# Optimization experiments

Hardware: AMD Instinct MI355X
Metric: run time of the kernel (lower is better)

Reference implementation:

```python
import jax, jax.numpy as jnp
import numpy as np

ENC_DIM = 256
DEC_HIDDEN = 128


def _lstm_cell(x, h, c, W_ih, W_hh, b_ih, b_hh):
    # gates: [B, 4H], PyTorch LSTMCell gate order: i, f, g, o
    gates = x @ W_ih.T + b_ih + h @ W_hh.T + b_hh
    i, f, g, o = jnp.split(gates, 4, axis=-1)
    i = jax.nn.sigmoid(i)
    f = jax.nn.sigmoid(f)
    g = jnp.tanh(g)
    o = jax.nn.sigmoid(o)
    c_new = f * c + i * g
    h_new = o * jnp.tanh(c_new)
    return h_new, c_new


def setup_inputs() -> dict:
    key = jax.random.key(0)
    ks = jax.random.split(key, 12)
    B, L, E, H = 256, 512, ENC_DIM, DEC_HIDDEN
    s_e = 1.0 / np.sqrt(H)
    inp = {
        "hist_ctx": jax.random.normal(ks[0], (B, L, E), dtype=jnp.float32),
        "fut_ctx": jax.random.normal(ks[1], (B, L, E), dtype=jnp.float32),
        "W_ih_h": jax.random.uniform(ks[2], (4 * H, E), jnp.float32, -s_e, s_e),
        "W_hh_h": jax.random.uniform(ks[3], (4 * H, H), jnp.float32, -s_e, s_e),
        "b_ih_h": jax.random.uniform(ks[4], (4 * H,), jnp.float32, -s_e, s_e),
        "b_hh_h": jax.random.uniform(ks[5], (4 * H,), jnp.float32, -s_e, s_e),
        "W_ih_f": jax.random.uniform(ks[6], (4 * H, E), jnp.float32, -s_e, s_e),
        "W_hh_f": jax.random.uniform(ks[7], (4 * H, H), jnp.float32, -s_e, s_e),
        "b_ih_f": jax.random.uniform(ks[8], (4 * H,), jnp.float32, -s_e, s_e),
        "b_hh_f": jax.random.uniform(ks[9], (4 * H,), jnp.float32, -s_e, s_e),
        "W_ffn": jax.random.uniform(ks[10], (1, 2 * H), jnp.float32, -1.0 / np.sqrt(2 * H), 1.0 / np.sqrt(2 * H)),
        "b_ffn": jax.random.uniform(ks[11], (1,), jnp.float32, -1.0 / np.sqrt(2 * H), 1.0 / np.sqrt(2 * H)),
    }
    return inp


def reference(hist_ctx, fut_ctx, W_ih_h, W_hh_h, b_ih_h, b_hh_h,
              W_ih_f, W_hh_f, b_ih_f, b_hh_f, W_ffn, b_ffn):
    B, L, _ = hist_ctx.shape
    H = W_hh_h.shape[1]
    h0 = jnp.zeros((B, H), dtype=hist_ctx.dtype)
    init = (h0, h0, h0, h0)  # h_h, c_h, h_f, c_f

    # time-major inputs for scan: [L, B, E]
    xs = (jnp.swapaxes(hist_ctx, 0, 1), jnp.swapaxes(fut_ctx, 0, 1))

    def step(carry, x):
        h_h, c_h, h_f, c_f = carry
        x_h, x_f = x
        h_h, c_h = _lstm_cell(x_h, h_h, c_h, W_ih_h, W_hh_h, b_ih_h, b_hh_h)
        h_f, c_f = _lstm_cell(x_f, h_f, c_f, W_ih_f, W_hh_f, b_ih_f, b_hh_f)
        comb = jnp.concatenate([h_h, h_f], axis=-1)  # [B, 2H]
        y_t = (comb @ W_ffn.T + b_ffn)[:, 0]          # [B]
        return (h_h, c_h, h_f, c_f), y_t

    _, ys = jax.lax.scan(step, init, xs)  # ys: [L, B]
    return jnp.swapaxes(ys, 0, 1)         # [B, L]
```

## Files before the change

### kernel.cpp

```cpp
#include <hip/hip_runtime.h>

#define B_ 256
#define L_ 512
#define E_ 256
#define H_ 128
#define G4_ 512
#define TC 16
#define NCH 32

typedef _Float16 half8  __attribute__((ext_vector_type(8)));
typedef float   float4v __attribute__((ext_vector_type(4)));
typedef int     int4v   __attribute__((ext_vector_type(4)));
typedef unsigned int uint32;

static constexpr size_t WT_OFF = 0;
static constexpr size_t WT_SZ  = (size_t)2 * 8 * 512 * 32 * 2;
static constexpr size_t WH_OFF = WT_OFF + WT_SZ;
static constexpr size_t WH_SZ  = (size_t)2 * 2 * 4 * 512 * 32 * 2;
static constexpr size_t YP_OFF = WH_OFF + WH_SZ;
static constexpr size_t YP_SZ  = (size_t)B_ * L_ * 4;
static constexpr size_t WS_NEEDED = YP_OFF + YP_SZ;

__device__ __forceinline__ int pk16(float lo, float hi) {
  return __builtin_bit_cast(int, __builtin_amdgcn_cvt_pkrtz(lo, hi));
}
__device__ __forceinline__ float sigf(float x) {
  return __builtin_amdgcn_rcpf(1.f + __builtin_amdgcn_exp2f(-1.44269504f * x));
}
__device__ __forceinline__ float tanhf_(float x) {
  return 1.f - 2.f * __builtin_amdgcn_rcpf(1.f + __builtin_amdgcn_exp2f(2.88539008f * x));
}

__global__ void prep(const float* __restrict__ WihH, const float* __restrict__ WihF,
                     const float* __restrict__ WhhH, const float* __restrict__ WhhF,
                     unsigned char* __restrict__ ws) {
  int id = blockIdx.x * 256 + threadIdx.x;
  if (id < 262144) {
    int lstm = id >> 17;
    int r = id & 131071;
    int kc = r >> 14;
    int r2 = r & 16383;
    int n = r2 >> 5, k5 = r2 & 31;
    const float* src = lstm ? WihF : WihH;
    ((_Float16*)(ws + WT_OFF))[id] = (_Float16)src[n * E_ + kc * 32 + k5];
  } else {
    int id2 = id - 262144;
    int lstm = id2 >> 17;
    int r = id2 & 131071;
    int sel = r >> 16;
    int r2 = r & 65535;
    int kc = r2 >> 14;
    int r3 = r2 & 16383;
    int n = r3 >> 5, k5 = r3 & 31;
    const float* src = lstm ? WhhF : WhhH;
    float wv = src[n * H_ + kc * 32 + k5];
    _Float16 hi = (_Float16)wv;
    _Float16 o = sel ? (_Float16)((wv - (float)hi) * 4096.f) : hi;
    ((_Float16*)(ws + WH_OFF))[id2] = o;
  }
}

__global__ __launch_bounds__(512, 2) void fused(
    const float* __restrict__ Xh, const float* __restrict__ Xf,
    const float* __restrict__ bihH, const float* __restrict__ bhhH,
    const float* __restrict__ bihF, const float* __restrict__ bhhF,
    const float* __restrict__ Wffn, unsigned char* __restrict__ ws,
    float* __restrict__ out) {
  const int bp = blockIdx.x, lstm = blockIdx.y;
  const int tid = threadIdx.x;
  const int w = tid >> 6, lane = tid & 63, quad = lane >> 4, l15 = lane & 15;
  __shared__ float GxL[TC * 2 * 512];
  __shared__ _Float16 hA2[2][512];
  __shared__ float hist[TC * 2 * 128];
  __shared__ float ybuf[2 * 512];

  const int u = w * 16 + l15;
  const int gk = u >> 3, jj = u & 7;
  const unsigned char* WH = ws + WH_OFF;
  half8 whh[2][4][4];
#pragma unroll
  for (int sel = 0; sel < 2; ++sel)
#pragma unroll
    for (int nt = 0; nt < 4; ++nt)
#pragma unroll
      for (int kc = 0; kc < 4; ++kc) {
        size_t byte =
            (size_t)(((lstm * 2 + sel) * 4 + kc) * 512 + (nt * 128 + u)) * 64 + quad * 16;
        whh[sel][nt][kc] = *(const half8*)(WH + byte);
      }
  float bias4[4];
#pragma unroll
  for (int nt = 0; nt < 4; ++nt) {
    int g = nt * 128 + u;
    bias4[nt] = lstm ? (bihF[g] + bhhF[g]) : (bihH[g] + bhhH[g]);
  }
  const float wf0 = Wffn[lstm * 128 + 2 * lane];
  const float wf1 = Wffn[lstm * 128 + 2 * lane + 1];
  const float* Xb0 = (lstm ? Xf : Xh) + (size_t)(2 * bp) * L_ * E_;
  const float* Xb1 = Xb0 + (size_t)L_ * E_;
  const unsigned char* WT = ws + WT_OFF + (size_t)lstm * 262144;
  float* yp1 = (float*)(ws + YP_OFF);
  float* ypout = (lstm == 0) ? (out + (size_t)(2 * bp) * L_) : (yp1 + (size_t)(2 * bp) * L_);

  float cst = 0.f;
  const float s_lo = 1.f / 4096.f;

  for (int ch = 0; ch < NCH; ++ch) {
    float4v ax[2][4];
#pragma unroll
    for (int mt = 0; mt < 2; ++mt)
#pragma unroll
      for (int nt = 0; nt < 4; ++nt) ax[mt][nt] = (float4v){0.f, 0.f, 0.f, 0.f};
#pragma unroll 2
    for (int kc = 0; kc < 8; ++kc) {
      const float* xa0 = Xb0 + (size_t)(ch * TC + l15) * E_ + kc * 32 + quad * 8;
      const float* xa1 = Xb1 + (size_t)(ch * TC + l15) * E_ + kc * 32 + quad * 8;
      float4v u0 = *(const float4v*)xa0, u1 = *(const float4v*)(xa0 + 4);
      float4v v0 = *(const float4v*)xa1, v1 = *(const float4v*)(xa1 + 4);
      int4v ai;
      ai[0] = pk16(u0[0], u0[1]); ai[1] = pk16(u0[2], u0[3]);
      ai[2] = pk16(u1[0], u1[1]); ai[3] = pk16(u1[2], u1[3]);
      half8 A0 = __builtin_bit_cast(half8, ai);
      ai[0] = pk16(v0[0], v0[1]); ai[1] = pk16(v0[2], v0[3]);
      ai[2] = pk16(v1[0], v1[1]); ai[3] = pk16(v1[2], v1[3]);
      half8 A1 = __builtin_bit_cast(half8, ai);
#pragma unroll
      for (int nt = 0; nt < 4; ++nt) {
        const unsigned char* bptr =
            WT + (size_t)kc * 32768 + (size_t)(nt * 128 + u) * 64 + quad * 16;
        half8 bf = *(const half8*)bptr;
        ax[0][nt] = __builtin_amdgcn_mfma_f32_16x16x32_f16(A0, bf, ax[0][nt], 0, 0, 0);
        ax[1][nt] = __builtin_amdgcn_mfma_f32_16x16x32_f16(A1, bf, ax[1][nt], 0, 0, 0);
      }
    }
#pragma unroll
    for (int mt = 0; mt < 2; ++mt)
#pragma unroll
      for (int nt = 0; nt < 4; ++nt) {
        int colg = nt * 128 + u;
        float bb = bias4[nt];
#pragma unroll
        for (int rg = 0; rg < 4; ++rg)
          GxL[((quad * 4 + rg) * 2 + mt) * 512 + colg] = ax[mt][nt][rg] + bb;
      }
    __syncthreads();

    for (int tl = 0; tl < TC; ++tl) {
      const int st = ch * TC + tl;
      const float* gp = &GxL[(tl * 2 + (quad & 1)) * 512 + u];
      float gx0 = gp[0], gx1 = gp[128], gx2 = gp[256], gx3 = gp[384];

      float4v r1[4], r2[4];
      if (st) {
        const _Float16* hAr = hA2[st & 1];
        half8 hfr[4];
#pragma unroll
        for (int kc = 0; kc < 4; ++kc)
          hfr[kc] = *(const half8*)&hAr[((kc * 4 + quad) * 4 + (l15 & 3)) * 8];
        const float4v z = (float4v){0.f, 0.f, 0.f, 0.f};
#pragma unroll
        for (int nt = 0; nt < 4; ++nt) {
          r1[nt] = __builtin_amdgcn_mfma_f32_16x16x32_f16(hfr[0], whh[0][nt][0], z, 0, 0, 0);
          r2[nt] = __builtin_amdgcn_mfma_f32_16x16x32_f16(hfr[0], whh[1][nt][0], z, 0, 0, 0);
        }
#pragma unroll
        for (int kc = 1; kc < 4; ++kc)
#pragma unroll
          for (int nt = 0; nt < 4; ++nt) {
            r1[nt] = __builtin_amdgcn_mfma_f32_16x16x32_f16(hfr[kc], whh[0][nt][kc], r1[nt], 0, 0, 0);
            r2[nt] = __builtin_amdgcn_mfma_f32_16x16x32_f16(hfr[kc], whh[1][nt][kc], r2[nt], 0, 0, 0);
          }
      } else {
#pragma unroll
        for (int nt = 0; nt < 4; ++nt) {
          r1[nt] = (float4v){0.f, 0.f, 0.f, 0.f};
          r2[nt] = (float4v){0.f, 0.f, 0.f, 0.f};
        }
      }
      if (quad < 2) {
        const int b = quad;
        const bool q1 = (b != 0);
        float p0 = (q1 ? r1[0][1] : r1[0][0]) + s_lo * ((q1 ? r1[0][3] : r1[0][2]) + (q1 ? r2[0][1] : r2[0][0])) + gx0;
        float p1 = (q1 ? r1[1][1] : r1[1][0]) + s_lo * ((q1 ? r1[1][3] : r1[1][2]) + (q1 ? r2[1][1] : r2[1][0])) + gx1;
        float p2 = (q1 ? r1[2][1] : r1[2][0]) + s_lo * ((q1 ? r1[2][3] : r1[2][2]) + (q1 ? r2[2][1] : r2[2][0])) + gx2;
        float p3 = (q1 ? r1[3][1] : r1[3][0]) + s_lo * ((q1 ? r1[3][3] : r1[3][2]) + (q1 ? r2[3][1] : r2[3][0])) + gx3;
        float iv = sigf(p0), fv = sigf(p1);
        float gg = tanhf_(p2), ov = sigf(p3);
        cst = fv * cst + iv * gg;
        float h = ov * tanhf_(cst);
        _Float16 hh = (_Float16)h;
        _Float16 hl = (_Float16)((h - (float)hh) * 4096.f);
        _Float16* hAw = hA2[(st + 1) & 1];
        hAw[(gk * 4 + b) * 8 + jj] = hh;
        hAw[(gk * 4 + 2 + b) * 8 + jj] = hl;
        hist[(tl * 2 + b) * 128 + u] = h;
      }
      __syncthreads();
    }

#pragma unroll
    for (int i = 0; i < 4; ++i) {
      int d = w * 4 + i;
      int tl = d >> 1, b = d & 1;
      float y = wf0 * hist[(tl * 2 + b) * 128 + 2 * lane] +
                wf1 * hist[(tl * 2 + b) * 128 + 2 * lane + 1];
      y += __shfl_xor(y, 1);
      y += __shfl_xor(y, 2);
      y += __shfl_xor(y, 4);
      y += __shfl_xor(y, 8);
      y += __shfl_xor(y, 16);
      y += __shfl_xor(y, 32);
      if (lane == 0) ybuf[b * 512 + ch * TC + tl] = y;
    }
    __syncthreads();
  }
  ypout[tid] = ybuf[tid];
  ypout[512 + tid] = ybuf[512 + tid];
}

__global__ __launch_bounds__(256) void combine(const unsigned char* __restrict__ ws,
                                               const float* __restrict__ bffn,
                                               float* __restrict__ out) {
  int i = blockIdx.x * 256 + threadIdx.x;
  const float* yp1 = (const float*)(ws + YP_OFF);
  out[i] = out[i] + yp1[i] + bffn[0];
}

extern "C" void kernel_launch(void* const* d_in, const int* in_sizes, int n_in,
                              void* d_out, int out_size, void* d_ws, size_t ws_size,
                              hipStream_t stream) {
  (void)in_sizes; (void)n_in; (void)out_size;
  const float* histX = (const float*)d_in[0];
  const float* futX  = (const float*)d_in[1];
  const float* WihH  = (const float*)d_in[2];
  const float* WhhH  = (const float*)d_in[3];
  const float* bihH  = (const float*)d_in[4];
  const float* bhhH  = (const float*)d_in[5];
  const float* WihF  = (const float*)d_in[6];
  const float* WhhF  = (const float*)d_in[7];
  const float* bihF  = (const float*)d_in[8];
  const float* bhhF  = (const float*)d_in[9];
  const float* Wffn  = (const float*)d_in[10];
  const float* bffn  = (const float*)d_in[11];
  unsigned char* ws = (unsigned char*)d_ws;
  float* out = (float*)d_out;

  if (ws_size < WS_NEEDED) return;

  prep<<<2048, 256, 0, stream>>>(WihH, WihF, WhhH, WhhF, ws);
  fused<<<dim3(B_ / 2, 2), 512, 0, stream>>>(histX, futX, bihH, bhhH, bihF, bhhF, Wffn, ws, out);
  combine<<<512, 256, 0, stream>>>(ws, bffn, out);
}
```

Baseline: 976.9 us.

## Software-pipeline next chunk's input projection into the recurrent timestep loop

The input-projection GEMM for chunk ch+1 is now spread across the 16 recurrent timesteps of chunk ch. Even steps issue the global loads for X and W_ih, and odd steps run the MFMAs, so the load latency and MFMA work hide behind the serial recurrence instead of stalling before each chunk. The GxL buffer gains a padded row stride (513) to reduce LDS bank conflicts. Launch bounds drop to one block per SM, which frees registers for the extra accumulators and prefetch buffers but lowers occupancy.

```diff
diff --git a/kernel.cpp b/kernel.cpp
--- a/kernel.cpp
+++ b/kernel.cpp
@@ -7,6 +7,7 @@
 #define G4_ 512
 #define TC 16
 #define NCH 32
+#define LDG 513
 
 typedef _Float16 half8  __attribute__((ext_vector_type(8)));
 typedef float   float4v __attribute__((ext_vector_type(4)));
@@ -60,7 +61,7 @@
   }
 }
 
-__global__ __launch_bounds__(512, 2) void fused(
+__global__ __launch_bounds__(512, 1) void fused(
     const float* __restrict__ Xh, const float* __restrict__ Xf,
     const float* __restrict__ bihH, const float* __restrict__ bhhH,
     const float* __restrict__ bihF, const float* __restrict__ bhhF,
@@ -69,7 +70,7 @@
   const int bp = blockIdx.x, lstm = blockIdx.y;
   const int tid = threadIdx.x;
   const int w = tid >> 6, lane = tid & 63, quad = lane >> 4, l15 = lane & 15;
-  __shared__ float GxL[TC * 2 * 512];
+  __shared__ float GxL[32 * LDG];
   __shared__ _Float16 hA2[2][512];
   __shared__ float hist[TC * 2 * 128];
   __shared__ float ybuf[2 * 512];
@@ -105,16 +106,16 @@
   float cst = 0.f;
   const float s_lo = 1.f / 4096.f;
 
-  for (int ch = 0; ch < NCH; ++ch) {
-    float4v ax[2][4];
+  {
+    float4v ax0[2][4];
 #pragma unroll
     for (int mt = 0; mt < 2; ++mt)
 #pragma unroll
-      for (int nt = 0; nt < 4; ++nt) ax[mt][nt] = (float4v){0.f, 0.f, 0.f, 0.f};
+      for (int nt = 0; nt < 4; ++nt) ax0[mt][nt] = (float4v){0.f, 0.f, 0.f, 0.f};
 #pragma unroll 2
     for (int kc = 0; kc < 8; ++kc) {
-      const float* xa0 = Xb0 + (size_t)(ch * TC + l15) * E_ + kc * 32 + quad * 8;
-      const float* xa1 = Xb1 + (size_t)(ch * TC + l15) * E_ + kc * 32 + quad * 8;
+      const float* xa0 = Xb0 + (size_t)l15 * E_ + kc * 32 + quad * 8;
+      const float* xa1 = Xb1 + (size_t)l15 * E_ + kc * 32 + quad * 8;
       float4v u0 = *(const float4v*)xa0, u1 = *(const float4v*)(xa0 + 4);
       float4v v0 = *(const float4v*)xa1, v1 = *(const float4v*)(xa1 + 4);
       int4v ai;
@@ -129,8 +130,8 @@
         const unsigned char* bptr =
             WT + (size_t)kc * 32768 + (size_t)(nt * 128 + u) * 64 + quad * 16;
         half8 bf = *(const half8*)bptr;
-        ax[0][nt] = __builtin_amdgcn_mfma_f32_16x16x32_f16(A0, bf, ax[0][nt], 0, 0, 0);
-        ax[1][nt] = __builtin_amdgcn_mfma_f32_16x16x32_f16(A1, bf, ax[1][nt], 0, 0, 0);
+        ax0[0][nt] = __builtin_amdgcn_mfma_f32_16x16x32_f16(A0, bf, ax0[0][nt], 0, 0, 0);
+        ax0[1][nt] = __builtin_amdgcn_mfma_f32_16x16x32_f16(A1, bf, ax0[1][nt], 0, 0, 0);
       }
     }
 #pragma unroll
@@ -141,13 +142,41 @@
         float bb = bias4[nt];
 #pragma unroll
         for (int rg = 0; rg < 4; ++rg)
-          GxL[((quad * 4 + rg) * 2 + mt) * 512 + colg] = ax[mt][nt][rg] + bb;
-      }
-    __syncthreads();
+          GxL[((quad * 4 + rg) * 2 + mt) * LDG + colg] = ax0[mt][nt][rg] + bb;
+      }
+  }
+  __syncthreads();
+
+  float4v ax[2][4];
+#pragma unroll
+  for (int mt = 0; mt < 2; ++mt)
+#pragma unroll
+    for (int nt = 0; nt < 4; ++nt) ax[mt][nt] = (float4v){0.f, 0.f, 0.f, 0.f};
+  float4v xu0, xu1, xv0, xv1;
+  half8 bfx0, bfx1, bfx2, bfx3;
+
+  for (int ch = 0; ch < NCH; ++ch) {
+    const bool hasx = (ch + 1 < NCH);
+    const float* Xn0 = Xb0 + (size_t)((ch + 1) * TC + l15) * E_;
+    const float* Xn1 = Xn0 + (size_t)L_ * E_;
 
     for (int tl = 0; tl < TC; ++tl) {
       const int st = ch * TC + tl;
-      const float* gp = &GxL[(tl * 2 + (quad & 1)) * 512 + u];
+
+      if (hasx && !(tl & 1)) {
+        const int k = tl >> 1;
+        const float* xa0 = Xn0 + k * 32 + quad * 8;
+        const float* xa1 = Xn1 + k * 32 + quad * 8;
+        xu0 = *(const float4v*)xa0; xu1 = *(const float4v*)(xa0 + 4);
+        xv0 = *(const float4v*)xa1; xv1 = *(const float4v*)(xa1 + 4);
+        const unsigned char* bb = WT + (size_t)k * 32768 + (size_t)u * 64 + quad * 16;
+        bfx0 = *(const half8*)(bb);
+        bfx1 = *(const half8*)(bb + 128 * 64);
+        bfx2 = *(const half8*)(bb + 256 * 64);
+        bfx3 = *(const half8*)(bb + 384 * 64);
+      }
+
+      const float* gp = &GxL[(tl * 2 + (quad & 1)) * LDG + u];
       float gx0 = gp[0], gx1 = gp[128], gx2 = gp[256], gx3 = gp[384];
 
       float4v r1[4], r2[4];
@@ -177,6 +206,25 @@
           r2[nt] = (float4v){0.f, 0.f, 0.f, 0.f};
         }
       }
+
+      if (hasx && (tl & 1)) {
+        int4v ai;
+        ai[0] = pk16(xu0[0], xu0[1]); ai[1] = pk16(xu0[2], xu0[3]);
+        ai[2] = pk16(xu1[0], xu1[1]); ai[3] = pk16(xu1[2], xu1[3]);
+        half8 A0 = __builtin_bit_cast(half8, ai);
+        ai[0] = pk16(xv0[0], xv0[1]); ai[1] = pk16(xv0[2], xv0[3]);
+        ai[2] = pk16(xv1[0], xv1[1]); ai[3] = pk16(xv1[2], xv1[3]);
+        half8 A1 = __builtin_bit_cast(half8, ai);
+        ax[0][0] = __builtin_amdgcn_mfma_f32_16x16x32_f16(A0, bfx0, ax[0][0], 0, 0, 0);
+        ax[1][0] = __builtin_amdgcn_mfma_f32_16x16x32_f16(A1, bfx0, ax[1][0], 0, 0, 0);
+        ax[0][1] = __builtin_amdgcn_mfma_f32_16x16x32_f16(A0, bfx1, ax[0][1], 0, 0, 0);
+        ax[1][1] = __builtin_amdgcn_mfma_f32_16x16x32_f16(A1, bfx1, ax[1][1], 0, 0, 0);
+        ax[0][2] = __builtin_amdgcn_mfma_f32_16x16x32_f16(A0, bfx2, ax[0][2], 0, 0, 0);
+        ax[1][2] = __builtin_amdgcn_mfma_f32_16x16x32_f16(A1, bfx2, ax[1][2], 0, 0, 0);
+        ax[0][3] = __builtin_amdgcn_mfma_f32_16x16x32_f16(A0, bfx3, ax[0][3], 0, 0, 0);
+        ax[1][3] = __builtin_amdgcn_mfma_f32_16x16x32_f16(A1, bfx3, ax[1][3], 0, 0, 0);
+      }
+
       if (quad < 2) {
         const int b = quad;
         const bool q1 = (b != 0);
@@ -211,6 +259,19 @@
       y += __shfl_xor(y, 16);
       y += __shfl_xor(y, 32);
       if (lane == 0) ybuf[b * 512 + ch * TC + tl] = y;
+    }
+    if (hasx) {
+#pragma unroll
+      for (int mt = 0; mt < 2; ++mt)
+#pragma unroll
+        for (int nt = 0; nt < 4; ++nt) {
+          int colg = nt * 128 + u;
+          float bb = bias4[nt];
+#pragma unroll
+          for (int rg = 0; rg < 4; ++rg)
+            GxL[((quad * 4 + rg) * 2 + mt) * LDG + colg] = ax[mt][nt][rg] + bb;
+          ax[mt][nt] = (float4v){0.f, 0.f, 0.f, 0.f};
+        }
     }
     __syncthreads();
   }
```

New measurement: 1.331 ms. 1.36x slower.

## Split gate activations across all four quads and pad gate-input LDS rows

Applied to the files above, without the earlier changes.

The recurrent step's four transcendental gate activations were computed only by the lower two quads. They are now spread so each lane computes two gates, and the results are exchanged with a cross-half shuffle, which shortens the serial critical path per timestep. The gate-input LDS buffer gets a padded row stride to avoid bank conflicts, and the step-zero branch is removed by zero-initialising the h buffer. Other changes: a partial unroll of the timestep loop, a float2 read in the output projection, and a renamed bias argument. The added shuffles and the extra padded LDS space may offset part of the gain.

```diff
diff --git a/kernel.cpp b/kernel.cpp
--- a/kernel.cpp
+++ b/kernel.cpp
@@ -7,6 +7,7 @@
 #define G4_ 512
 #define TC 16
 #define NCH 32
+#define LDG 513
 
 typedef _Float16 half8  __attribute__((ext_vector_type(8)));
 typedef float   float4v __attribute__((ext_vector_type(4)));
@@ -69,7 +70,7 @@
   const int bp = blockIdx.x, lstm = blockIdx.y;
   const int tid = threadIdx.x;
   const int w = tid >> 6, lane = tid & 63, quad = lane >> 4, l15 = lane & 15;
-  __shared__ float GxL[TC * 2 * 512];
+  __shared__ float GxL[32 * LDG];
   __shared__ _Float16 hA2[2][512];
   __shared__ float hist[TC * 2 * 128];
   __shared__ float ybuf[2 * 512];
@@ -104,6 +105,8 @@
 
   float cst = 0.f;
   const float s_lo = 1.f / 4096.f;
+
+  hA2[0][tid] = (_Float16)0.f;
 
   for (int ch = 0; ch < NCH; ++ch) {
     float4v ax[2][4];
@@ -141,59 +144,60 @@
         float bb = bias4[nt];
 #pragma unroll
         for (int rg = 0; rg < 4; ++rg)
-          GxL[((quad * 4 + rg) * 2 + mt) * 512 + colg] = ax[mt][nt][rg] + bb;
+          GxL[((quad * 4 + rg) * 2 + mt) * LDG + colg] = ax[mt][nt][rg] + bb;
       }
     __syncthreads();
 
+#pragma unroll 4
     for (int tl = 0; tl < TC; ++tl) {
       const int st = ch * TC + tl;
-      const float* gp = &GxL[(tl * 2 + (quad & 1)) * 512 + u];
-      float gx0 = gp[0], gx1 = gp[128], gx2 = gp[256], gx3 = gp[384];
-
+      const bool hi2 = (quad >= 2);
+      const int bq = quad & 1;
+
+      const float* gp = &GxL[(tl * 2 + bq) * LDG + u + (hi2 ? 256 : 0)];
+      float gxA = gp[0], gxB = gp[128];
+
+      const _Float16* hAr = hA2[st & 1];
+      half8 hfr[4];
+#pragma unroll
+      for (int kc = 0; kc < 4; ++kc)
+        hfr[kc] = *(const half8*)&hAr[((kc * 4 + quad) * 4 + (l15 & 3)) * 8];
+      const float4v z = (float4v){0.f, 0.f, 0.f, 0.f};
       float4v r1[4], r2[4];
-      if (st) {
-        const _Float16* hAr = hA2[st & 1];
-        half8 hfr[4];
-#pragma unroll
-        for (int kc = 0; kc < 4; ++kc)
-          hfr[kc] = *(const half8*)&hAr[((kc * 4 + quad) * 4 + (l15 & 3)) * 8];
-        const float4v z = (float4v){0.f, 0.f, 0.f, 0.f};
+#pragma unroll
+      for (int nt = 0; nt < 4; ++nt) {
+        r1[nt] = __builtin_amdgcn_mfma_f32_16x16x32_f16(hfr[0], whh[0][nt][0], z, 0, 0, 0);
+        r2[nt] = __builtin_amdgcn_mfma_f32_16x16x32_f16(hfr[0], whh[1][nt][0], z, 0, 0, 0);
+      }
+#pragma unroll
+      for (int kc = 1; kc < 4; ++kc)
 #pragma unroll
         for (int nt = 0; nt < 4; ++nt) {
-          r1[nt] = __builtin_amdgcn_mfma_f32_16x16x32_f16(hfr[0], whh[0][nt][0], z, 0, 0, 0);
-          r2[nt] = __builtin_amdgcn_mfma_f32_16x16x32_f16(hfr[0], whh[1][nt][0], z, 0, 0, 0);
+          r1[nt] = __builtin_amdgcn_mfma_f32_16x16x32_f16(hfr[kc], whh[0][nt][kc], r1[nt], 0, 0, 0);
+          r2[nt] = __builtin_amdgcn_mfma_f32_16x16x32_f16(hfr[kc], whh[1][nt][kc], r2[nt], 0, 0, 0);
         }
-#pragma unroll
-        for (int kc = 1; kc < 4; ++kc)
-#pragma unroll
-          for (int nt = 0; nt < 4; ++nt) {
-            r1[nt] = __builtin_amdgcn_mfma_f32_16x16x32_f16(hfr[kc], whh[0][nt][kc], r1[nt], 0, 0, 0);
-            r2[nt] = __builtin_amdgcn_mfma_f32_16x16x32_f16(hfr[kc], whh[1][nt][kc], r2[nt], 0, 0, 0);
-          }
-      } else {
-#pragma unroll
-        for (int nt = 0; nt < 4; ++nt) {
-          r1[nt] = (float4v){0.f, 0.f, 0.f, 0.f};
-          r2[nt] = (float4v){0.f, 0.f, 0.f, 0.f};
-        }
-      }
+
+      float hiA  = hi2 ? (bq ? r1[2][1] : r1[2][0]) : (bq ? r1[0][1] : r1[0][0]);
+      float loA  = hi2 ? (bq ? r1[2][3] : r1[2][2]) : (bq ? r1[0][3] : r1[0][2]);
+      float wlA  = hi2 ? (bq ? r2[2][1] : r2[2][0]) : (bq ? r2[0][1] : r2[0][0]);
+      float hiB  = hi2 ? (bq ? r1[3][1] : r1[3][0]) : (bq ? r1[1][1] : r1[1][0]);
+      float loB  = hi2 ? (bq ? r1[3][3] : r1[3][2]) : (bq ? r1[1][3] : r1[1][2]);
+      float wlB  = hi2 ? (bq ? r2[3][1] : r2[3][0]) : (bq ? r2[1][1] : r2[1][0]);
+      float pA = hiA + s_lo * (loA + wlA) + gxA;
+      float pB = hiB + s_lo * (loB + wlB) + gxB;
+      float vA = hi2 ? tanhf_(pA) : sigf(pA);
+      float vB = sigf(pB);
+      float gg = __shfl_xor(vA, 32);
+      float oo = __shfl_xor(vB, 32);
       if (quad < 2) {
-        const int b = quad;
-        const bool q1 = (b != 0);
-        float p0 = (q1 ? r1[0][1] : r1[0][0]) + s_lo * ((q1 ? r1[0][3] : r1[0][2]) + (q1 ? r2[0][1] : r2[0][0])) + gx0;
-        float p1 = (q1 ? r1[1][1] : r1[1][0]) + s_lo * ((q1 ? r1[1][3] : r1[1][2]) + (q1 ? r2[1][1] : r2[1][0])) + gx1;
-        float p2 = (q1 ? r1[2][1] : r1[2][0]) + s_lo * ((q1 ? r1[2][3] : r1[2][2]) + (q1 ? r2[2][1] : r2[2][0])) + gx2;
-        float p3 = (q1 ? r1[3][1] : r1[3][0]) + s_lo * ((q1 ? r1[3][3] : r1[3][2]) + (q1 ? r2[3][1] : r2[3][0])) + gx3;
-        float iv = sigf(p0), fv = sigf(p1);
-        float gg = tanhf_(p2), ov = sigf(p3);
-        cst = fv * cst + iv * gg;
-        float h = ov * tanhf_(cst);
+        cst = vB * cst + vA * gg;
+        float h = oo * tanhf_(cst);
         _Float16 hh = (_Float16)h;
         _Float16 hl = (_Float16)((h - (float)hh) * 4096.f);
         _Float16* hAw = hA2[(st + 1) & 1];
-        hAw[(gk * 4 + b) * 8 + jj] = hh;
-        hAw[(gk * 4 + 2 + b) * 8 + jj] = hl;
-        hist[(tl * 2 + b) * 128 + u] = h;
+        hAw[(gk * 4 + bq) * 8 + jj] = hh;
+        hAw[(gk * 4 + 2 + bq) * 8 + jj] = hl;
+        hist[(tl * 2 + bq) * 128 + u] = h;
       }
       __syncthreads();
     }
@@ -202,8 +206,8 @@
     for (int i = 0; i < 4; ++i) {
       int d = w * 4 + i;
       int tl = d >> 1, b = d & 1;
-      float y = wf0 * hist[(tl * 2 + b) * 128 + 2 * lane] +
-                wf1 * hist[(tl * 2 + b) * 128 + 2 * lane + 1];
+      float2 hv = *(const float2*)&hist[(tl * 2 + b) * 128 + 2 * lane];
+      float y = wf0 * hv.x + wf1 * hv.y;
       y += __shfl_xor(y, 1);
       y += __shfl_xor(y, 2);
       y += __shfl_xor(y, 4);
@@ -239,7 +243,7 @@
   const float* WihF  = (const float*)d_in[6];
   const float* WhhF  = (const float*)d_in[7];
   const float* bihF  = (const float*)d_in[8];
-  const float* bhhF  = (const float*)d_in[9];
+  const float* bihF2 = (const float*)d_in[9];
   const float* Wffn  = (const float*)d_in[10];
   const float* bffn  = (const float*)d_in[11];
   unsigned char* ws = (unsigned char*)d_ws;
@@ -248,6 +252,6 @@
   if (ws_size < WS_NEEDED) return;
 
   prep<<<2048, 256, 0, stream>>>(WihH, WihF, WhhH, WhhF, ws);
-  fused<<<dim3(B_ / 2, 2), 512, 0, stream>>>(histX, futX, bihH, bhhH, bihF, bhhF, Wffn, ws, out);
+  fused<<<dim3(B_ / 2, 2), 512, 0, stream>>>(histX, futX, bihH, bhhH, bihF, bihF2, Wffn, ws, out);
   combine<<<512, 256, 0, stream>>>(ws, bffn, out);
 }
```

Result: slower. 1.009 ms (+3.3%).

## Prefetch next chunk's inputs into LDS during recurrence steps, pad gate buffer

Applied to the files above, without the earlier changes.

The next chunk's fp32 inputs are loaded from global memory and packed to fp16 into an LDS buffer while the current chunk's serial recurrent steps run, spread across the first 8 steps. The input projection then reads its A operands from LDS instead of issuing global loads in front of the MFMAs. Other changes: the gate buffer row stride is padded to 513 to reduce LDS bank conflicts, the step-0 special case is removed by zeroing the h buffer, and __syncthreads is replaced with a raw s_waitcnt lgkmcnt plus s_barrier. The launch bound drops to one block per CU, which gives more registers but less occupancy, and the raw barrier depends on global loads not needing to be waited on at that point.

```diff
diff --git a/kernel.cpp b/kernel.cpp
--- a/kernel.cpp
+++ b/kernel.cpp
@@ -7,11 +7,11 @@
 #define G4_ 512
 #define TC 16
 #define NCH 32
+#define LDG 513
 
 typedef _Float16 half8  __attribute__((ext_vector_type(8)));
 typedef float   float4v __attribute__((ext_vector_type(4)));
 typedef int     int4v   __attribute__((ext_vector_type(4)));
-typedef unsigned int uint32;
 
 static constexpr size_t WT_OFF = 0;
 static constexpr size_t WT_SZ  = (size_t)2 * 8 * 512 * 32 * 2;
@@ -29,6 +29,9 @@
 }
 __device__ __forceinline__ float tanhf_(float x) {
   return 1.f - 2.f * __builtin_amdgcn_rcpf(1.f + __builtin_amdgcn_exp2f(2.88539008f * x));
+}
+__device__ __forceinline__ void step_barrier() {
+  asm volatile("s_waitcnt lgkmcnt(0)\n\ts_barrier" ::: "memory");
 }
 
 __global__ void prep(const float* __restrict__ WihH, const float* __restrict__ WihF,
@@ -60,7 +63,7 @@
   }
 }
 
-__global__ __launch_bounds__(512, 2) void fused(
+__global__ __launch_bounds__(512, 1) void fused(
     const float* __restrict__ Xh, const float* __restrict__ Xf,
     const float* __restrict__ bihH, const float* __restrict__ bhhH,
     const float* __restrict__ bihF, const float* __restrict__ bhhF,
@@ -69,10 +72,11 @@
   const int bp = blockIdx.x, lstm = blockIdx.y;
   const int tid = threadIdx.x;
   const int w = tid >> 6, lane = tid & 63, quad = lane >> 4, l15 = lane & 15;
-  __shared__ float GxL[TC * 2 * 512];
+  __shared__ float GxL[32 * LDG];
   __shared__ _Float16 hA2[2][512];
   __shared__ float hist[TC * 2 * 128];
   __shared__ float ybuf[2 * 512];
+  __shared__ _Float16 XS[2][16][264];
 
   const int u = w * 16 + l15;
   const int gk = u >> 3, jj = u & 7;
@@ -105,7 +109,28 @@
   float cst = 0.f;
   const float s_lo = 1.f / 4096.f;
 
+  hA2[0][tid] = (_Float16)0.f;
+
+  {
+    float2 pv[8];
+#pragma unroll
+    for (int r = 0; r < 8; ++r) {
+      int f = r * 1024 + tid * 2;
+      int sb = f >> 12, stt = (f >> 8) & 15, se = f & 255;
+      pv[r] = *(const float2*)((sb ? Xb1 : Xb0) + (size_t)stt * E_ + se);
+    }
+#pragma unroll
+    for (int r = 0; r < 8; ++r) {
+      int f = r * 1024 + tid * 2;
+      int sb = f >> 12, stt = (f >> 8) & 15, se = f & 255;
+      *(int*)&XS[sb][stt][se] = pk16(pv[r].x, pv[r].y);
+    }
+  }
+  __syncthreads();
+
   for (int ch = 0; ch < NCH; ++ch) {
+    const bool stg = (ch + 1 < NCH);
+
     float4v ax[2][4];
 #pragma unroll
     for (int mt = 0; mt < 2; ++mt)
@@ -113,17 +138,8 @@
       for (int nt = 0; nt < 4; ++nt) ax[mt][nt] = (float4v){0.f, 0.f, 0.f, 0.f};
 #pragma unroll 2
     for (int kc = 0; kc < 8; ++kc) {
-      const float* xa0 = Xb0 + (size_t)(ch * TC + l15) * E_ + kc * 32 + quad * 8;
-      const float* xa1 = Xb1 + (size_t)(ch * TC + l15) * E_ + kc * 32 + quad * 8;
-      float4v u0 = *(const float4v*)xa0, u1 = *(const float4v*)(xa0 + 4);
-      float4v v0 = *(const float4v*)xa1, v1 = *(const float4v*)(xa1 + 4);
-      int4v ai;
-      ai[0] = pk16(u0[0], u0[1]); ai[1] = pk16(u0[2], u0[3]);
-      ai[2] = pk16(u1[0], u1[1]); ai[3] = pk16(u1[2], u1[3]);
-      half8 A0 = __builtin_bit_cast(half8, ai);
-      ai[0] = pk16(v0[0], v0[1]); ai[1] = pk16(v0[2], v0[3]);
-      ai[2] = pk16(v1[0], v1[1]); ai[3] = pk16(v1[2], v1[3]);
-      half8 A1 = __builtin_bit_cast(half8, ai);
+      half8 A0 = *(const half8*)&XS[0][l15][kc * 32 + quad * 8];
+      half8 A1 = *(const half8*)&XS[1][l15][kc * 32 + quad * 8];
 #pragma unroll
       for (int nt = 0; nt < 4; ++nt) {
         const unsigned char* bptr =
@@ -141,42 +157,48 @@
         float bb = bias4[nt];
 #pragma unroll
         for (int rg = 0; rg < 4; ++rg)
-          GxL[((quad * 4 + rg) * 2 + mt) * 512 + colg] = ax[mt][nt][rg] + bb;
+          GxL[((quad * 4 + rg) * 2 + mt) * LDG + colg] = ax[mt][nt][rg] + bb;
       }
     __syncthreads();
 
+#pragma unroll 4
     for (int tl = 0; tl < TC; ++tl) {
       const int st = ch * TC + tl;
-      const float* gp = &GxL[(tl * 2 + (quad & 1)) * 512 + u];
+
+      float2 xv;
+      int sb = 0, stt = 0, se = 0;
+      const bool dostg = stg && (tl < 8);
+      if (dostg) {
+        int f = tl * 1024 + tid * 2;
+        sb = f >> 12; stt = (f >> 8) & 15; se = f & 255;
+        xv = *(const float2*)((sb ? Xb1 : Xb0) + (size_t)((ch + 1) * TC + stt) * E_ + se);
+      }
+
+      const float* gp = &GxL[(tl * 2 + (quad & 1)) * LDG + u];
       float gx0 = gp[0], gx1 = gp[128], gx2 = gp[256], gx3 = gp[384];
 
+      const _Float16* hAr = hA2[st & 1];
+      half8 hfr[4];
+#pragma unroll
+      for (int kc = 0; kc < 4; ++kc)
+        hfr[kc] = *(const half8*)&hAr[((kc * 4 + quad) * 4 + (l15 & 3)) * 8];
+      const float4v z = (float4v){0.f, 0.f, 0.f, 0.f};
       float4v r1[4], r2[4];
-      if (st) {
-        const _Float16* hAr = hA2[st & 1];
-        half8 hfr[4];
-#pragma unroll
-        for (int kc = 0; kc < 4; ++kc)
-          hfr[kc] = *(const half8*)&hAr[((kc * 4 + quad) * 4 + (l15 & 3)) * 8];
-        const float4v z = (float4v){0.f, 0.f, 0.f, 0.f};
+#pragma unroll
+      for (int nt = 0; nt < 4; ++nt) {
+        r1[nt] = __builtin_amdgcn_mfma_f32_16x16x32_f16(hfr[0], whh[0][nt][0], z, 0, 0, 0);
+        r2[nt] = __builtin_amdgcn_mfma_f32_16x16x32_f16(hfr[0], whh[1][nt][0], z, 0, 0, 0);
+      }
+#pragma unroll
+      for (int kc = 1; kc < 4; ++kc)
 #pragma unroll
         for (int nt = 0; nt < 4; ++nt) {
-          r1[nt] = __builtin_amdgcn_mfma_f32_16x16x32_f16(hfr[0], whh[0][nt][0], z, 0, 0, 0);
-          r2[nt] = __builtin_amdgcn_mfma_f32_16x16x32_f16(hfr[0], whh[1][nt][0], z, 0, 0, 0);
+          r1[nt] = __builtin_amdgcn_mfma_f32_16x16x32_f16(hfr[kc], whh[0][nt][kc], r1[nt], 0, 0, 0);
+          r2[nt] = __builtin_amdgcn_mfma_f32_16x16x32_f16(hfr[kc], whh[1][nt][kc], r2[nt], 0, 0, 0);
         }
-#pragma unroll
-        for (int kc = 1; kc < 4; ++kc)
-#pragma unroll
-          for (int nt = 0; nt < 4; ++nt) {
-            r1[nt] = __builtin_amdgcn_mfma_f32_16x16x32_f16(hfr[kc], whh[0][nt][kc], r1[nt], 0, 0, 0);
-            r2[nt] = __builtin_amdgcn_mfma_f32_16x16x32_f16(hfr[kc], whh[1][nt][kc], r2[nt], 0, 0, 0);
-          }
-      } else {
-#pragma unroll
-        for (int nt = 0; nt < 4; ++nt) {
-          r1[nt] = (float4v){0.f, 0.f, 0.f, 0.f};
-          r2[nt] = (float4v){0.f, 0.f, 0.f, 0.f};
-        }
-      }
+
+      if (dostg) *(int*)&XS[sb][stt][se] = pk16(xv.x, xv.y);
+
       if (quad < 2) {
         const int b = quad;
         const bool q1 = (b != 0);
@@ -195,15 +217,15 @@
         hAw[(gk * 4 + 2 + b) * 8 + jj] = hl;
         hist[(tl * 2 + b) * 128 + u] = h;
       }
-      __syncthreads();
+      step_barrier();
     }
 
 #pragma unroll
     for (int i = 0; i < 4; ++i) {
       int d = w * 4 + i;
       int tl = d >> 1, b = d & 1;
-      float y = wf0 * hist[(tl * 2 + b) * 128 + 2 * lane] +
-                wf1 * hist[(tl * 2 + b) * 128 + 2 * lane + 1];
+      float2 hv = *(const float2*)&hist[(tl * 2 + b) * 128 + 2 * lane];
+      float y = wf0 * hv.x + wf1 * hv.y;
       y += __shfl_xor(y, 1);
       y += __shfl_xor(y, 2);
       y += __shfl_xor(y, 4);
```

New measurement: 794.4 us. 18.7% less time.
